# Kernel tuning notes

Measured on AMD Instinct MI355X. Metric: run time of the kernel, lower is better.

The kernel has to match this reference:

```python
import jax, jax.numpy as jnp
import numpy as np

HEADS = 6
K = 3       # kernel_size
PAD = 1     # padding (stride = 1, so AvgPool is identity and h=H, w=W)


def setup_inputs() -> dict:
    key = jax.random.key(0)
    ks = jax.random.split(key, 6)
    B, H, W, C = 8, 56, 56, 192
    k4h = (K ** 4) * HEADS  # 486
    s = 0.02
    return {
        "x":  jax.random.normal(ks[0], (B, H, W, C), jnp.float32),
        # weights stored as (in, out), i.e. transpose of torch nn.Linear.weight
        "Wv": jax.random.normal(ks[1], (C, C), jnp.float32) * s,
        "Wa": jax.random.normal(ks[2], (C, k4h), jnp.float32) * s,
        "ba": jnp.zeros((k4h,), jnp.float32),
        "Wp": jax.random.normal(ks[3], (C, C), jnp.float32) * s,
        "bp": jnp.zeros((C,), jnp.float32),
    }


def _outlook(x, Wv, Wa, ba, Wp, bp):
    B, H, W, C = x.shape
    hd = C // HEADS
    scale = hd ** (-0.5)
    k2 = K * K
    hw = H * W

    # v projection (no bias), to NCHW
    v = jnp.einsum("bhwc,cd->bdhw", x, Wv)                       # [B,C,H,W]

    # unfold: extract k x k local windows (same ordering as nn.Unfold: C, ki, kj)
    vp = jnp.pad(v, ((0, 0), (0, 0), (PAD, PAD), (PAD, PAD)))
    patches = jnp.stack(
        [vp[:, :, i:i + H, j:j + W] for i in range(K) for j in range(K)],
        axis=2,
    )                                                            # [B,C,k2,H,W]
    v = patches.reshape(B, HEADS, hd, k2, hw).transpose(0, 1, 4, 3, 2)  # [B,h,hw,k2,hd]

    # attention weights: dense predicted per location (pool is identity, stride=1)
    a = x.reshape(B, hw, C) @ Wa + ba                            # [B,hw,heads*k2*k2]
    a = a.reshape(B, hw, HEADS, k2, k2).transpose(0, 2, 1, 3, 4)  # [B,h,hw,k2,k2]
    a = jax.nn.softmax(a * scale, axis=-1)

    out = jnp.einsum("bnpkq,bnpqd->bnpkd", a, v)                 # [B,h,hw,k2,hd]

    # fold (col2im): scatter-add overlapping windows back, stride=1
    cols = out.transpose(0, 1, 4, 3, 2).reshape(B, C, K, K, H, W)
    acc = jnp.zeros((B, C, H + 2 * PAD, W + 2 * PAD), x.dtype)
    for i in range(K):
        for j in range(K):
            acc = acc.at[:, :, i:i + H, j:j + W].add(cols[:, :, i, j])
    y = acc[:, :, PAD:PAD + H, PAD:PAD + W].transpose(0, 2, 3, 1)  # [B,H,W,C]

    return y @ Wp + bp


def reference(x, Wv, Wa, ba, Wp, bp):
    return _outlook(x, Wv, Wa, ba, Wp, bp)
```

## Files before the change

kernel.cpp:

```cpp
#include <hip/hip_runtime.h>
#include <hip/hip_bf16.h>
#include <cstdint>

#define DI __device__ __forceinline__

typedef __attribute__((ext_vector_type(8))) short short8;
typedef __attribute__((ext_vector_type(4))) float f32x4;

DI float bflo(uint32_t u) { return __builtin_bit_cast(float, (uint32_t)(u << 16)); }
DI float bfhi(uint32_t u) { return __builtin_bit_cast(float, (uint32_t)(u & 0xffff0000u)); }
DI float bf2f(uint16_t u) { return __builtin_bit_cast(float, (uint32_t)((uint32_t)u << 16)); }
DI uint32_t cvtpk(float lo, float hi) {
    uint32_t r;
    asm("v_cvt_pk_bf16_f32 %0, %1, %2" : "=v"(r) : "v"(lo), "v"(hi));
    return r;
}

DI void gload16(const void* g, void* s) {
    __builtin_amdgcn_global_load_lds(
        (const __attribute__((address_space(1))) uint32_t*)g,
        (__attribute__((address_space(3))) uint32_t*)s, 16, 0, 0);
}

DI int xcd_swizzle(int orig, int nwg) {
    const int q = nwg >> 3, r = nwg & 7;
    const int x = orig & 7, i = orig >> 3;
    return (x < r ? x * (q + 1) : r * (q + 1) + (x - r) * q) + i;
}

constexpr int BATCH = 8, HH_IMG = 56, WW_IMG = 56, C = 192;
constexpr int HEADS = 6, HD = 32, NA = 486;
constexpr int MROWS = BATCH * HH_IMG * WW_IMG;
constexpr int KK = 192;
constexpr int TILE_B = 49152;

__global__ __launch_bounds__(256) void prep_wt(const float* __restrict__ Wv,
                                               const float* __restrict__ Wa,
                                               const float* __restrict__ Wp,
                                               uint8_t* __restrict__ WT) {
    const int tid = blockIdx.x * 256 + threadIdx.x;
    const int s = tid % 24, rem = tid / 24;
    const int p = rem & 127, tile = rem >> 7;
    const int lc = (p >> 5) * 32 + 2 * (p & 15) + ((p >> 4) & 1);
    const int u  = (tile < 6 ? tile : tile - 6) * 128 + lc;

    const float* src = nullptr; int nc = 0, col = 0;
    if (tile < 6) {
        if (u < 192)      { src = Wv; nc = 192; col = u; }
        else if (u < 678) { src = Wa; nc = NA;  col = u - 192; }
    } else {
        if (u < 192)      { src = Wp; nc = 192; col = u; }
    }

    const int k0 = s * 8;
    uint32_t d[4];
#pragma unroll
    for (int e = 0; e < 4; ++e) {
        const float f0 = src ? src[(size_t)(k0 + 2 * e) * nc + col]     : 0.f;
        const float f1 = src ? src[(size_t)(k0 + 2 * e + 1) * nc + col] : 0.f;
        d[e] = cvtpk(f0, f1);
    }
    const int sb = (s * 16) ^ ((p & 7) << 4);
    *(uint4*)(WT + (size_t)tile * TILE_B + p * 384 + sb) =
        make_uint4(d[0], d[1], d[2], d[3]);
}

template <bool A_BF16, bool OUT_DUAL, int NT>
__global__ __launch_bounds__(256, 2) void gemm128(
    const void* __restrict__ Ap,
    const uint8_t* __restrict__ WT,
    uint16_t* __restrict__ vOut, uint16_t* __restrict__ alogOut,
    const float* __restrict__ bias,
    float* __restrict__ outf) {
    __shared__ __align__(16) uint8_t sm[TILE_B];
    const int t    = threadIdx.x;
    const int wgid = xcd_swizzle(blockIdx.x, gridDim.x);
    const int mg   = wgid / NT, ti = wgid - mg * NT;
    const int m0   = mg * 128;
    const int l    = t & 63, wid = t >> 6;
    const int wr   = wid >> 1, wc = wid & 1;
    const int lr   = l & 15, lg = l >> 4;

    if (A_BF16) {
        const uint8_t* src = (const uint8_t*)Ap + (size_t)m0 * 384;
#pragma unroll
        for (int i = 0; i < 12; ++i) {
            const int off = wid * 12288 + i * 1024;
            gload16(src + off + l * 16, sm + off);
        }
        __syncthreads();
    } else {
        const float* A = (const float*)Ap;
#pragma unroll
        for (int i = 0; i < 12; ++i) {
            const int f = t + i * 256;
            const int m = f / 24, cb = (f % 24) * 16;
            const int k = cb >> 1;
            const float4 v0 = *(const float4*)(A + (size_t)(m0 + m) * KK + k);
            const float4 v1 = *(const float4*)(A + (size_t)(m0 + m) * KK + k + 4);
            uint4 o;
            o.x = cvtpk(v0.x, v0.y); o.y = cvtpk(v0.z, v0.w);
            o.z = cvtpk(v1.x, v1.y); o.w = cvtpk(v1.z, v1.w);
            *(uint4*)(sm + m * 384 + (cb ^ ((m & 7) << 4))) = o;
        }
        __syncthreads();
    }

    short8 aR[6][4];
#pragma unroll
    for (int ks = 0; ks < 6; ++ks)
#pragma unroll
        for (int mr = 0; mr < 4; ++mr) {
            const int row = wr * 64 + mr * 16 + lr;
            aR[ks][mr] = *(const short8*)(sm + row * 384 +
                          ((ks * 64 + lg * 16) ^ ((row & 7) << 4)));
        }
    __syncthreads();

    {
        const uint8_t* wt = WT + (size_t)ti * TILE_B;
#pragma unroll
        for (int i = 0; i < 12; ++i) {
            const int off = wid * 12288 + i * 1024;
            gload16(wt + off + l * 16, sm + off);
        }
    }
    __syncthreads();

    f32x4 acc[4][4];
#pragma unroll
    for (int mr = 0; mr < 4; ++mr)
#pragma unroll
        for (int nr = 0; nr < 4; ++nr) acc[mr][nr] = f32x4{0.f, 0.f, 0.f, 0.f};
#pragma unroll
    for (int ks = 0; ks < 6; ++ks) {
        const int cb = ks * 64 + lg * 16;
        short8 b[4];
#pragma unroll
        for (int nr = 0; nr < 4; ++nr) {
            const int rn = wc * 64 + nr * 16 + lr;
            b[nr] = *(const short8*)(sm + rn * 384 + (cb ^ ((rn & 7) << 4)));
        }
#pragma unroll
        for (int mr = 0; mr < 4; ++mr)
#pragma unroll
            for (int nr = 0; nr < 4; ++nr)
                acc[mr][nr] = __builtin_amdgcn_mfma_f32_16x16x32_bf16(
                    aR[ks][mr], b[nr], acc[mr][nr], 0, 0, 0);
    }

    const int gcol0 = ti * 128 + wc * 64;
#pragma unroll
    for (int pr = 0; pr < 2; ++pr) {
        if (OUT_DUAL) {
            const bool isv = gcol0 < 192;
            uint16_t* dst = isv ? vOut : alogOut;
            const int nc  = isv ? 192 : NA;
            const int c   = (isv ? gcol0 : gcol0 - 192) + pr * 32 + 2 * lr;
            if (c < nc) {
                const float be = isv ? 0.f : bias[c];
                const float bo = isv ? 0.f : bias[c + 1];
#pragma unroll
                for (int mr = 0; mr < 4; ++mr) {
                    const size_t rb = (size_t)(m0 + wr * 64 + mr * 16 + lg * 4);
#pragma unroll
                    for (int j = 0; j < 4; ++j)
                        *(uint32_t*)(dst + (rb + j) * nc + c) =
                            cvtpk(acc[mr][2 * pr][j] + be, acc[mr][2 * pr + 1][j] + bo);
                }
            }
        } else {
            const int c = gcol0 + pr * 32 + 2 * lr;
            if (c < 192) {
                const float be = bias[c], bo = bias[c + 1];
#pragma unroll
                for (int mr = 0; mr < 4; ++mr) {
                    const size_t rb = (size_t)(m0 + wr * 64 + mr * 16 + lg * 4);
#pragma unroll
                    for (int j = 0; j < 4; ++j)
                        *(float2*)(outf + (rb + j) * 192 + c) =
                            make_float2(acc[mr][2 * pr][j] + be,
                                        acc[mr][2 * pr + 1][j] + bo);
                }
            }
        }
    }
}

constexpr int TH = 4, TW = 8;
constexpr int HALO_W = TW + 4;
constexpr int VSTR = C + 8;

__global__ __launch_bounds__(192) void attn_fold25(const uint16_t* __restrict__ v,
                                                   const uint16_t* __restrict__ alog,
                                                   uint16_t* __restrict__ ypre) {
    __shared__ uint16_t vl[96][VSTR];
    const int b   = blockIdx.z;
    const int ty0 = blockIdx.y * TH, tx0 = blockIdx.x * TW;
    const int t   = threadIdx.x;

#pragma unroll
    for (int it = 0; it < 12; ++it) {
        const int f  = t + it * 192;
        const int px = f / 24, c8 = (f % 24) * 8;
        const int hy = px / HALO_W, hx = px % HALO_W;
        const int y = ty0 + hy - 2, x = tx0 + hx - 2;
        uint4 val = make_uint4(0u, 0u, 0u, 0u);
        if ((unsigned)y < HH_IMG && (unsigned)x < WW_IMG)
            val = *(const uint4*)&v[(((size_t)b * HH_IMG + y) * WW_IMG + x) * C + c8];
        *(uint4*)&vl[px][c8] = val;
    }

    const int n   = t % HEADS, pxl = t / HEADS;
    const int py  = pxl / TW, px_ = pxl % TW;
    const int Py  = ty0 + py, Px = tx0 + px_;
    const float scl2 = 0.17677669529663687f * 1.4426950408889634f;

    float cw[5][5] = {};
#pragma unroll
    for (int i = 0; i < 3; ++i)
#pragma unroll
        for (int j = 0; j < 3; ++j) {
            const int sy = Py - i + 1, sx = Px - j + 1;
            if ((unsigned)sy < HH_IMG && (unsigned)sx < WW_IMG) {
                const uint16_t* ap = alog + (((size_t)b * HH_IMG + sy) * WW_IMG + sx) * NA
                                   + n * 81 + (i * 3 + j) * 9;
                float w[9], s = 0.f;
#pragma unroll
                for (int q = 0; q < 9; ++q) {
                    w[q] = __builtin_amdgcn_exp2f(bf2f(ap[q]) * scl2);
                    s += w[q];
                }
                const float inv = __builtin_amdgcn_rcpf(s);
#pragma unroll
                for (int qi = 0; qi < 3; ++qi)
#pragma unroll
                    for (int qj = 0; qj < 3; ++qj)
                        cw[qi - i + 2][qj - j + 2] += w[qi * 3 + qj] * inv;
            }
        }
    __syncthreads();

    float acc[HD] = {};
#pragma unroll
    for (int dy = 0; dy < 5; ++dy)
#pragma unroll
        for (int dx = 0; dx < 5; ++dx) {
            const float wq = cw[dy][dx];
            const uint16_t* vp = &vl[(py + dy) * HALO_W + (px_ + dx)][n * HD];
#pragma unroll
            for (int v8 = 0; v8 < 4; ++v8) {
                const uint4 raw = *(const uint4*)&vp[v8 * 8];
                const uint32_t r0 = raw.x, r1 = raw.y, r2 = raw.z, r3 = raw.w;
                acc[v8*8+0] = fmaf(wq, bflo(r0), acc[v8*8+0]);
                acc[v8*8+1] = fmaf(wq, bfhi(r0), acc[v8*8+1]);
                acc[v8*8+2] = fmaf(wq, bflo(r1), acc[v8*8+2]);
                acc[v8*8+3] = fmaf(wq, bfhi(r1), acc[v8*8+3]);
                acc[v8*8+4] = fmaf(wq, bflo(r2), acc[v8*8+4]);
                acc[v8*8+5] = fmaf(wq, bfhi(r2), acc[v8*8+5]);
                acc[v8*8+6] = fmaf(wq, bflo(r3), acc[v8*8+6]);
                acc[v8*8+7] = fmaf(wq, bfhi(r3), acc[v8*8+7]);
            }
        }

    const size_t Pidx = ((size_t)b * HH_IMG + Py) * WW_IMG + Px;
    uint8_t* op = (uint8_t*)ypre + Pidx * 384;
    const int key = ((int)Pidx & 7) << 4;
#pragma unroll
    for (int d = 0; d < HD; d += 2)
        *(uint32_t*)(op + ((n * 64 + d * 2) ^ key)) = cvtpk(acc[d], acc[d + 1]);
}

extern "C" void kernel_launch(void* const* d_in, const int* in_sizes, int n_in,
                              void* d_out, int out_size, void* d_ws, size_t ws_size,
                              hipStream_t stream) {
    const float* x  = (const float*)d_in[0];
    const float* Wv = (const float*)d_in[1];
    const float* Wa = (const float*)d_in[2];
    const float* ba = (const float*)d_in[3];
    const float* Wp = (const float*)d_in[4];
    const float* bp = (const float*)d_in[5];
    float* out = (float*)d_out;

    uint16_t* v    = (uint16_t*)d_ws;
    uint16_t* alog = v + (size_t)MROWS * C;
    uint16_t* ypre = alog + (size_t)MROWS * NA;
    uint8_t*  WT   = (uint8_t*)(ypre + (size_t)MROWS * C);

    prep_wt<<<96, 256, 0, stream>>>(Wv, Wa, Wp, WT);
    gemm128<false, true, 6><<<(MROWS / 128) * 6, 256, 0, stream>>>(
        x, WT, v, alog, ba, nullptr);
    attn_fold25<<<dim3(WW_IMG / TW, HH_IMG / TH, BATCH), dim3(192), 0, stream>>>(
        v, alog, ypre);
    gemm128<true, false, 2><<<(MROWS / 128) * 2, 256, 0, stream>>>(
        ypre, WT + 6 * (size_t)TILE_B, nullptr, nullptr, bp, out);
}
```

Measured before the change: 67.78 us.

## Pre-convert x to bf16 MFMA fragment panels and load A directly into registers

After: 61.64 us. 9.1% less time.

```diff
diff --git a/kernel.cpp b/kernel.cpp
--- a/kernel.cpp
+++ b/kernel.cpp
@@ -15,13 +15,11 @@
     asm("v_cvt_pk_bf16_f32 %0, %1, %2" : "=v"(r) : "v"(lo), "v"(hi));
     return r;
 }
-
 DI void gload16(const void* g, void* s) {
     __builtin_amdgcn_global_load_lds(
         (const __attribute__((address_space(1))) uint32_t*)g,
         (__attribute__((address_space(3))) uint32_t*)s, 16, 0, 0);
 }
-
 DI int xcd_swizzle(int orig, int nwg) {
     const int q = nwg >> 3, r = nwg & 7;
     const int x = orig & 7, i = orig >> 3;
@@ -32,42 +30,60 @@
 constexpr int HEADS = 6, HD = 32, NA = 486;
 constexpr int MROWS = BATCH * HH_IMG * WW_IMG;
 constexpr int KK = 192;
-constexpr int TILE_B = 49152;
-
-__global__ __launch_bounds__(256) void prep_wt(const float* __restrict__ Wv,
-                                               const float* __restrict__ Wa,
-                                               const float* __restrict__ Wp,
-                                               uint8_t* __restrict__ WT) {
-    const int tid = blockIdx.x * 256 + threadIdx.x;
-    const int s = tid % 24, rem = tid / 24;
-    const int p = rem & 127, tile = rem >> 7;
-    const int lc = (p >> 5) * 32 + 2 * (p & 15) + ((p >> 4) & 1);
-    const int u  = (tile < 6 ? tile : tile - 6) * 128 + lc;
-
-    const float* src = nullptr; int nc = 0, col = 0;
-    if (tile < 6) {
-        if (u < 192)      { src = Wv; nc = 192; col = u; }
-        else if (u < 678) { src = Wa; nc = NA;  col = u - 192; }
+constexpr int TILE_B  = 49152;
+constexpr int PANEL_B = 49152;
+
+
+__global__ __launch_bounds__(256) void prep_all(const float* __restrict__ x,
+                                                const float* __restrict__ Wv,
+                                                const float* __restrict__ Wa,
+                                                const float* __restrict__ Wp,
+                                                uint8_t* __restrict__ xbf,
+                                                uint8_t* __restrict__ WT) {
+    const int bid = blockIdx.x;
+    if (bid < 2352) {
+        const int g = bid * 256 + threadIdx.x;
+        const int m = g / 24, cc = g % 24;
+        const int ks = cc >> 2, lg = cc & 3;
+        const float* src = x + (size_t)m * KK + cc * 8;
+        const float4 v0 = *(const float4*)src;
+        const float4 v1 = *(const float4*)(src + 4);
+        uint4 o;
+        o.x = cvtpk(v0.x, v0.y); o.y = cvtpk(v0.z, v0.w);
+        o.z = cvtpk(v1.x, v1.y); o.w = cvtpk(v1.z, v1.w);
+        const size_t off = (size_t)(m >> 7) * PANEL_B +
+                           ((((m >> 4) & 7) * 6 + ks) * 64 + (lg << 4) + (m & 15)) * 16;
+        *(uint4*)(xbf + off) = o;
     } else {
-        if (u < 192)      { src = Wp; nc = 192; col = u; }
-    }
-
-    const int k0 = s * 8;
-    uint32_t d[4];
-#pragma unroll
-    for (int e = 0; e < 4; ++e) {
-        const float f0 = src ? src[(size_t)(k0 + 2 * e) * nc + col]     : 0.f;
-        const float f1 = src ? src[(size_t)(k0 + 2 * e + 1) * nc + col] : 0.f;
-        d[e] = cvtpk(f0, f1);
-    }
-    const int sb = (s * 16) ^ ((p & 7) << 4);
-    *(uint4*)(WT + (size_t)tile * TILE_B + p * 384 + sb) =
-        make_uint4(d[0], d[1], d[2], d[3]);
-}
-
-template <bool A_BF16, bool OUT_DUAL, int NT>
-__global__ __launch_bounds__(256, 2) void gemm128(
-    const void* __restrict__ Ap,
+        const int tid = (bid - 2352) * 256 + threadIdx.x;
+        const int s = tid % 24, rem = tid / 24;
+        const int p = rem & 127, tile = rem >> 7;
+        const int lc = (p >> 5) * 32 + 2 * (p & 15) + ((p >> 4) & 1);
+        const int u  = (tile < 6 ? tile : tile - 6) * 128 + lc;
+        const float* src = nullptr; int nc = 0, col = 0;
+        if (tile < 6) {
+            if (u < 192)      { src = Wv; nc = 192; col = u; }
+            else if (u < 678) { src = Wa; nc = NA;  col = u - 192; }
+        } else {
+            if (u < 192)      { src = Wp; nc = 192; col = u; }
+        }
+        const int k0 = s * 8;
+        uint32_t d[4];
+#pragma unroll
+        for (int e = 0; e < 4; ++e) {
+            const float f0 = src ? src[(size_t)(k0 + 2 * e) * nc + col]     : 0.f;
+            const float f1 = src ? src[(size_t)(k0 + 2 * e + 1) * nc + col] : 0.f;
+            d[e] = cvtpk(f0, f1);
+        }
+        const int sb = (s * 16) ^ ((p & 7) << 4);
+        *(uint4*)(WT + (size_t)tile * TILE_B + p * 384 + sb) =
+            make_uint4(d[0], d[1], d[2], d[3]);
+    }
+}
+
+template <bool OUT_DUAL, int NT>
+__global__ __launch_bounds__(256, 2) void gemm_fr(
+    const uint8_t* __restrict__ Afr,
     const uint8_t* __restrict__ WT,
     uint16_t* __restrict__ vOut, uint16_t* __restrict__ alogOut,
     const float* __restrict__ bias,
@@ -81,50 +97,22 @@
     const int wr   = wid >> 1, wc = wid & 1;
     const int lr   = l & 15, lg = l >> 4;
 
-    if (A_BF16) {
-        const uint8_t* src = (const uint8_t*)Ap + (size_t)m0 * 384;
-#pragma unroll
-        for (int i = 0; i < 12; ++i) {
-            const int off = wid * 12288 + i * 1024;
-            gload16(src + off + l * 16, sm + off);
-        }
-        __syncthreads();
-    } else {
-        const float* A = (const float*)Ap;
-#pragma unroll
-        for (int i = 0; i < 12; ++i) {
-            const int f = t + i * 256;
-            const int m = f / 24, cb = (f % 24) * 16;
-            const int k = cb >> 1;
-            const float4 v0 = *(const float4*)(A + (size_t)(m0 + m) * KK + k);
-            const float4 v1 = *(const float4*)(A + (size_t)(m0 + m) * KK + k + 4);
-            uint4 o;
-            o.x = cvtpk(v0.x, v0.y); o.y = cvtpk(v0.z, v0.w);
-            o.z = cvtpk(v1.x, v1.y); o.w = cvtpk(v1.z, v1.w);
-            *(uint4*)(sm + m * 384 + (cb ^ ((m & 7) << 4))) = o;
-        }
-        __syncthreads();
-    }
-
+    const uint8_t* wt = WT + (size_t)ti * TILE_B;
+#pragma unroll
+    for (int i = 0; i < 12; ++i) {
+        const int off = wid * 12288 + i * 1024;
+        gload16(wt + off + l * 16, sm + off);
+    }
+
+    const uint8_t* ap = Afr + (size_t)mg * PANEL_B;
     short8 aR[6][4];
 #pragma unroll
     for (int ks = 0; ks < 6; ++ks)
 #pragma unroll
         for (int mr = 0; mr < 4; ++mr) {
-            const int row = wr * 64 + mr * 16 + lr;
-            aR[ks][mr] = *(const short8*)(sm + row * 384 +
-                          ((ks * 64 + lg * 16) ^ ((row & 7) << 4)));
-        }
-    __syncthreads();
-
-    {
-        const uint8_t* wt = WT + (size_t)ti * TILE_B;
-#pragma unroll
-        for (int i = 0; i < 12; ++i) {
-            const int off = wid * 12288 + i * 1024;
-            gload16(wt + off + l * 16, sm + off);
-        }
-    }
+            const int r = wr * 4 + mr;
+            aR[ks][mr] = *(const short8*)(ap + (size_t)(((r * 6 + ks) * 64) + l) * 16);
+        }
     __syncthreads();
 
     f32x4 acc[4][4];
@@ -193,7 +181,7 @@
 
 __global__ __launch_bounds__(192) void attn_fold25(const uint16_t* __restrict__ v,
                                                    const uint16_t* __restrict__ alog,
-                                                   uint16_t* __restrict__ ypre) {
+                                                   uint8_t* __restrict__ ypre) {
     __shared__ uint16_t vl[96][VSTR];
     const int b   = blockIdx.z;
     const int ty0 = blockIdx.y * TH, tx0 = blockIdx.x * TW;
@@ -263,12 +251,18 @@
             }
         }
 
-    const size_t Pidx = ((size_t)b * HH_IMG + Py) * WW_IMG + Px;
-    uint8_t* op = (uint8_t*)ypre + Pidx * 384;
-    const int key = ((int)Pidx & 7) << 4;
-#pragma unroll
-    for (int d = 0; d < HD; d += 2)
-        *(uint32_t*)(op + ((n * 64 + d * 2) ^ key)) = cvtpk(acc[d], acc[d + 1]);
+    const int Pidx = (b * HH_IMG + Py) * WW_IMG + Px;
+    uint8_t* pb = ypre + (size_t)(Pidx >> 7) * PANEL_B +
+                  ((((Pidx >> 4) & 7) * 6 + n) * 64 + (Pidx & 15)) * 16;
+#pragma unroll
+    for (int g2 = 0; g2 < 4; ++g2) {
+        uint4 o;
+        o.x = cvtpk(acc[g2 * 8 + 0], acc[g2 * 8 + 1]);
+        o.y = cvtpk(acc[g2 * 8 + 2], acc[g2 * 8 + 3]);
+        o.z = cvtpk(acc[g2 * 8 + 4], acc[g2 * 8 + 5]);
+        o.w = cvtpk(acc[g2 * 8 + 6], acc[g2 * 8 + 7]);
+        *(uint4*)(pb + g2 * 256) = o;
+    }
 }
 
 extern "C" void kernel_launch(void* const* d_in, const int* in_sizes, int n_in,
@@ -284,14 +278,15 @@
 
     uint16_t* v    = (uint16_t*)d_ws;
     uint16_t* alog = v + (size_t)MROWS * C;
-    uint16_t* ypre = alog + (size_t)MROWS * NA;
-    uint8_t*  WT   = (uint8_t*)(ypre + (size_t)MROWS * C);
-
-    prep_wt<<<96, 256, 0, stream>>>(Wv, Wa, Wp, WT);
-    gemm128<false, true, 6><<<(MROWS / 128) * 6, 256, 0, stream>>>(
-        x, WT, v, alog, ba, nullptr);
+    uint8_t*  ypre = (uint8_t*)(alog + (size_t)MROWS * NA);
+    uint8_t*  WT   = ypre + (size_t)(MROWS / 128) * PANEL_B;
+    uint8_t*  xbf  = WT + 8 * (size_t)TILE_B;
+
+    prep_all<<<2448, 256, 0, stream>>>(x, Wv, Wa, Wp, xbf, WT);
+    gemm_fr<true, 6><<<(MROWS / 128) * 6, 256, 0, stream>>>(
+        xbf, WT, v, alog, ba, nullptr);
     attn_fold25<<<dim3(WW_IMG / TW, HH_IMG / TH, BATCH), dim3(192), 0, stream>>>(
         v, alog, ypre);
-    gemm128<true, false, 2><<<(MROWS / 128) * 2, 256, 0, stream>>>(
+    gemm_fr<false, 2><<<(MROWS / 128) * 2, 256, 0, stream>>>(
         ypre, WT + 6 * (size_t)TILE_B, nullptr, nullptr, bp, out);
 }
```
